# Performance work log

Measured on AMD Instinct MI355X. Metric: run time of the kernel, lower is better.

## Reference

```python
import jax, jax.numpy as jnp
import numpy as np

NUM_CLASSES = 8192
FEAT_DIM = 2048
BATCH = 4096


def setup_inputs() -> dict:
    key = jax.random.key(0)
    k1, k2, k3 = jax.random.split(key, 3)
    x = jax.random.normal(k1, (BATCH, FEAT_DIM), dtype=jnp.float32)
    labels = jax.random.randint(k2, (BATCH,), 0, NUM_CLASSES, dtype=jnp.int64)
    centers = jax.random.normal(k3, (NUM_CLASSES, FEAT_DIM), dtype=jnp.float32)
    return {"x": x, "labels": labels, "centers": centers}


def reference(x, labels, centers):
    # Original builds a dense [B, C] squared-distance matrix via addmm, then
    # per-row masks out the single entry at column labels[i]. Mathematically
    # dist_i = ||x_i||^2 + ||c_{y_i}||^2 - 2 <x_i, c_{y_i}>, so we gather the
    # label's center row directly instead of materializing the full distmat.
    c_sel = centers[labels]                              # [B, D] gather
    x_sq = jnp.sum(x * x, axis=1)                        # [B]
    c_sq = jnp.sum(c_sel * c_sel, axis=1)                # [B]
    cross = jnp.sum(x * c_sel, axis=1)                   # [B]
    dist = x_sq + c_sq - 2.0 * cross                     # [B]
    dist = jnp.clip(dist, 1e-12, 1e12)                   # clamp(min=1e-12, max=1e12)
    return jnp.mean(dist)                                # weights=None path -> mean
```

## Files before the change

### kernel.cpp

```cpp
#include <hip/hip_runtime.h>

#define BATCH 4096
#define FEAT  2048

typedef float f32x4 __attribute__((ext_vector_type(4)));

__global__ __launch_bounds__(256) void center_loss_rows(
        const float* __restrict__ x,
        const int*   __restrict__ labels,
        const float* __restrict__ centers,
        float*       __restrict__ row_dist) {
    const int row = blockIdx.x;
    const int t   = threadIdx.x;

    const int lbl = labels[row];
    const f32x4* __restrict__ xr = (const f32x4*)(x + (size_t)row * FEAT) + t;
    const f32x4* __restrict__ cr = (const f32x4*)(centers + (size_t)lbl * FEAT) + t;

    f32x4 xv0 = __builtin_nontemporal_load(xr);
    f32x4 xv1 = __builtin_nontemporal_load(xr + 256);
    f32x4 cv0 = cr[0];
    f32x4 cv1 = cr[256];

    float p = 0.f;
    p += xv0.x * xv0.x + xv0.y * xv0.y + xv0.z * xv0.z + xv0.w * xv0.w;
    p += xv1.x * xv1.x + xv1.y * xv1.y + xv1.z * xv1.z + xv1.w * xv1.w;
    p += cv0.x * cv0.x + cv0.y * cv0.y + cv0.z * cv0.z + cv0.w * cv0.w;
    p += cv1.x * cv1.x + cv1.y * cv1.y + cv1.z * cv1.z + cv1.w * cv1.w;
    p -= 2.0f * (xv0.x * cv0.x + xv0.y * cv0.y + xv0.z * cv0.z + xv0.w * cv0.w +
                 xv1.x * cv1.x + xv1.y * cv1.y + xv1.z * cv1.z + xv1.w * cv1.w);

#pragma unroll
    for (int off = 32; off > 0; off >>= 1)
        p += __shfl_down(p, off, 64);

    __shared__ float sw[4];
    const int wave = t >> 6;
    if ((t & 63) == 0) sw[wave] = p;
    __syncthreads();

    if (t == 0) {
        float d = sw[0] + sw[1] + sw[2] + sw[3];
        d = fminf(fmaxf(d, 1e-12f), 1e12f);
        row_dist[row] = d;
    }
}

__global__ __launch_bounds__(256) void reduce_mean_kernel(
        const float* __restrict__ row_dist,
        float*       __restrict__ out) {
    const int t = threadIdx.x;
    float s = 0.f;
#pragma unroll
    for (int i = 0; i < BATCH / 256; ++i)
        s += row_dist[t + i * 256];

#pragma unroll
    for (int off = 32; off > 0; off >>= 1)
        s += __shfl_down(s, off, 64);

    __shared__ float sw[4];
    const int wave = t >> 6;
    if ((t & 63) == 0) sw[wave] = s;
    __syncthreads();

    if (t == 0)
        out[0] = (sw[0] + sw[1] + sw[2] + sw[3]) * (1.0f / (float)BATCH);
}

extern "C" void kernel_launch(void* const* d_in, const int* in_sizes, int n_in,
                              void* d_out, int out_size, void* d_ws, size_t ws_size,
                              hipStream_t stream) {
    const float* x       = (const float*)d_in[0];
    const int*   labels  = (const int*)d_in[1];
    const float* centers = (const float*)d_in[2];
    float* out = (float*)d_out;
    float* row_dist = (float*)d_ws;

    center_loss_rows<<<BATCH, 256, 0, stream>>>(x, labels, centers, row_dist);
    reduce_mean_kernel<<<1, 256, 0, stream>>>(row_dist, out);
}
```

Measured before the change: 16.48 us.

## Map one wavefront per row and compute distance as squared difference

Each 64-lane wavefront now handles a full row, with 8 vector loads per operand per lane, so the LDS cross-wave reduction and __syncthreads go away and the grid is a quarter the size. The distance is computed as sum((x-c)^2) instead of expanding the three norm terms, which cuts arithmetic and may change rounding slightly. The final mean reduction reads row distances with float4 loads. More loads are in flight per lane, at the cost of more registers and fewer blocks.

```diff
diff --git a/kernel.cpp b/kernel.cpp
--- a/kernel.cpp
+++ b/kernel.cpp
@@ -10,38 +10,35 @@
         const int*   __restrict__ labels,
         const float* __restrict__ centers,
         float*       __restrict__ row_dist) {
-    const int row = blockIdx.x;
-    const int t   = threadIdx.x;
+    const int wave = threadIdx.x >> 6;
+    const int lane = threadIdx.x & 63;
+    const int row  = (blockIdx.x << 2) | wave;
 
     const int lbl = labels[row];
-    const f32x4* __restrict__ xr = (const f32x4*)(x + (size_t)row * FEAT) + t;
-    const f32x4* __restrict__ cr = (const f32x4*)(centers + (size_t)lbl * FEAT) + t;
+    const f32x4* __restrict__ xr = (const f32x4*)(x + (size_t)row * FEAT) + lane;
+    const f32x4* __restrict__ cr = (const f32x4*)(centers + (size_t)lbl * FEAT) + lane;
 
-    f32x4 xv0 = __builtin_nontemporal_load(xr);
-    f32x4 xv1 = __builtin_nontemporal_load(xr + 256);
-    f32x4 cv0 = cr[0];
-    f32x4 cv1 = cr[256];
+    f32x4 xv[8], cv[8];
+#pragma unroll
+    for (int i = 0; i < 8; ++i)
+        xv[i] = __builtin_nontemporal_load(xr + (i << 6));
+#pragma unroll
+    for (int i = 0; i < 8; ++i)
+        cv[i] = cr[i << 6];
 
     float p = 0.f;
-    p += xv0.x * xv0.x + xv0.y * xv0.y + xv0.z * xv0.z + xv0.w * xv0.w;
-    p += xv1.x * xv1.x + xv1.y * xv1.y + xv1.z * xv1.z + xv1.w * xv1.w;
-    p += cv0.x * cv0.x + cv0.y * cv0.y + cv0.z * cv0.z + cv0.w * cv0.w;
-    p += cv1.x * cv1.x + cv1.y * cv1.y + cv1.z * cv1.z + cv1.w * cv1.w;
-    p -= 2.0f * (xv0.x * cv0.x + xv0.y * cv0.y + xv0.z * cv0.z + xv0.w * cv0.w +
-                 xv1.x * cv1.x + xv1.y * cv1.y + xv1.z * cv1.z + xv1.w * cv1.w);
+#pragma unroll
+    for (int i = 0; i < 8; ++i) {
+        f32x4 d = xv[i] - cv[i];
+        p += d.x * d.x + d.y * d.y + d.z * d.z + d.w * d.w;
+    }
 
 #pragma unroll
     for (int off = 32; off > 0; off >>= 1)
         p += __shfl_down(p, off, 64);
 
-    __shared__ float sw[4];
-    const int wave = t >> 6;
-    if ((t & 63) == 0) sw[wave] = p;
-    __syncthreads();
-
-    if (t == 0) {
-        float d = sw[0] + sw[1] + sw[2] + sw[3];
-        d = fminf(fmaxf(d, 1e-12f), 1e12f);
+    if (lane == 0) {
+        float d = fminf(fmaxf(p, 1e-12f), 1e12f);
         row_dist[row] = d;
     }
 }
@@ -50,10 +47,14 @@
         const float* __restrict__ row_dist,
         float*       __restrict__ out) {
     const int t = threadIdx.x;
+    const f32x4* __restrict__ rd = (const f32x4*)row_dist;
+
     float s = 0.f;
 #pragma unroll
-    for (int i = 0; i < BATCH / 256; ++i)
-        s += row_dist[t + i * 256];
+    for (int i = 0; i < BATCH / 4 / 256; ++i) {
+        f32x4 v = rd[t + i * 256];
+        s += v.x + v.y + v.z + v.w;
+    }
 
 #pragma unroll
     for (int off = 32; off > 0; off >>= 1)
@@ -77,6 +78,6 @@
     float* out = (float*)d_out;
     float* row_dist = (float*)d_ws;
 
-    center_loss_rows<<<BATCH, 256, 0, stream>>>(x, labels, centers, row_dist);
+    center_loss_rows<<<BATCH / 4, 256, 0, stream>>>(x, labels, centers, row_dist);
     reduce_mean_kernel<<<1, 256, 0, stream>>>(row_dist, out);
 }
```

New measurement: 16.00 us. 1.03x faster.
